# Performance work log

Measured on AMD Instinct MI355X. Metric: run time of the kernel, lower is better.

## Reference

```python
import jax, jax.numpy as jnp
import numpy as np

N, E = 50000, 800000
HID, EDGE_DIM, HEADS = 128, 16, 4
C = HID // HEADS  # 32
NEG_SLOPE = 0.2  # GATv2Conv default negative_slope


def setup_inputs() -> dict:
    key = jax.random.key(0)
    ks = jax.random.split(key, 16)
    def glorot(k, shape):
        fan_in = shape[0]
        return jax.random.normal(k, shape, jnp.float32) / np.sqrt(fan_in)
    return {
        "x": jax.random.normal(ks[0], (N, HID), jnp.float32),
        "edge_index": jax.random.randint(ks[1], (2, E), 0, N, jnp.int64 if jax.config.jax_enable_x64 else jnp.int32),
        "edge_attr": jax.random.normal(ks[2], (E, EDGE_DIM), jnp.float32),
        # GATv2Conv params (lin_l, lin_r with bias; lin_edge bias-free; att; final bias)
        "Wl": glorot(ks[3], (HID, HID)),
        "bl": jnp.zeros((HID,), jnp.float32),
        "Wr": glorot(ks[4], (HID, HID)),
        "br": jnp.zeros((HID,), jnp.float32),
        "We": glorot(ks[5], (EDGE_DIM, HID)),
        "att": glorot(ks[6], (HEADS, C)),
        "bias_gat": jnp.zeros((HID,), jnp.float32),
        # RMSNorm weights
        "w_norm1": jnp.ones((HID,), jnp.float32),
        "w_norm2": jnp.ones((HID,), jnp.float32),
        # FFN params
        "ffn_w1": glorot(ks[7], (HID, 4 * HID)),
        "ffn_b1": jnp.zeros((4 * HID,), jnp.float32),
        "ffn_w2": glorot(ks[8], (4 * HID, HID)),
        "ffn_b2": jnp.zeros((HID,), jnp.float32),
    }


def rmsnorm(x, w):
    # torch.nn.RMSNorm with eps=None -> eps = finfo(dtype).eps
    eps = jnp.finfo(x.dtype).eps
    ms = jnp.mean(x * x, axis=-1, keepdims=True)
    return x * jax.lax.rsqrt(ms + eps) * w


def gatv2_conv(x, edge_index, edge_attr, Wl, bl, Wr, br, We, att, bias_gat):
    n = x.shape[0]
    h, c = att.shape
    xl = (x @ Wl + bl).reshape(n, h, c)   # source-side transform (x_j)
    xr = (x @ Wr + br).reshape(n, h, c)   # target-side transform (x_i)
    src, dst = edge_index[0], edge_index[1]
    e = (edge_attr @ We).reshape(-1, h, c)
    m = xl[src] + xr[dst] + e                       # [E, H, C] per-edge message pre-activation
    s = jnp.where(m > 0, m, NEG_SLOPE * m)          # LeakyReLU(0.2)
    logits = jnp.einsum('ehc,hc->eh', s, att)       # [E, H]
    # scatter-softmax over edges grouped by target node
    lmax = jax.ops.segment_max(logits, dst, num_segments=n)
    ex = jnp.exp(logits - lmax[dst])
    den = jax.ops.segment_sum(ex, dst, num_segments=n)
    alpha = ex / (den[dst] + 1e-16)                 # PyG softmax denominator guard
    out = jax.ops.segment_sum(alpha[..., None] * xl[src], dst, num_segments=n)
    return out.reshape(n, h * c) + bias_gat


def reference(x, edge_index, edge_attr, Wl, bl, Wr, br, We, att, bias_gat,
              w_norm1, w_norm2, ffn_w1, ffn_b1, ffn_w2, ffn_b2):
    x_attn = gatv2_conv(x, edge_index, edge_attr, Wl, bl, Wr, br, We, att, bias_gat)
    h = rmsnorm(x + x_attn, w_norm1)
    f = jax.nn.gelu(h @ ffn_w1 + ffn_b1, approximate=False) @ ffn_w2 + ffn_b2
    return rmsnorm(h + f, w_norm2)
```

## Files before the change

### kernel.cpp

```cpp
#include <hip/hip_runtime.h>

#define NN 50000
#define EE 800000

typedef unsigned short u16;

#define OFF_GAT  0u
#define OFF_XLB  6400000u
#define OFF_XRB  9600000u
#define OFF_SE   12800000u
#define OFF_CNT  14400000u
#define OFF_OFS  14450000u
#define OFF_H    6400000u
#define OFF_HB   12800000u
#define OFF_WLRT 16000000u
#define OFF_W1T  16016384u
#define OFF_W2T  16049152u

#define RMS_EPS 1.1920928955078125e-7f

typedef float f32x4v __attribute__((ext_vector_type(4)));
typedef short s16x8 __attribute__((ext_vector_type(8)));

__device__ __forceinline__ f32x4v mfma16(s16x8 a, s16x8 b, f32x4v c) {
  return __builtin_amdgcn_mfma_f32_16x16x32_bf16(a, b, c, 0, 0, 0);
}
__device__ __forceinline__ u16 f2b(float f) {
  unsigned int u = __float_as_uint(f);
  unsigned int r = (u + 0x7fffu + ((u >> 16) & 1u)) >> 16;
  return (u16)r;
}
__device__ __forceinline__ float b2f(u16 u) {
  union { float f; unsigned int i; } x; x.i = ((unsigned int)u) << 16; return x.f;
}
__device__ __forceinline__ s16x8 ld_bf16x8_f32(const float* __restrict__ p) {
  float4 v0 = *(const float4*)p;
  float4 v1 = *(const float4*)(p + 4);
  s16x8 r;
  r[0] = (short)f2b(v0.x); r[1] = (short)f2b(v0.y);
  r[2] = (short)f2b(v0.z); r[3] = (short)f2b(v0.w);
  r[4] = (short)f2b(v1.x); r[5] = (short)f2b(v1.y);
  r[6] = (short)f2b(v1.z); r[7] = (short)f2b(v1.w);
  return r;
}
__device__ __forceinline__ float readlane_f32(float v, int lane) {
  return __int_as_float(__builtin_amdgcn_readlane(__float_as_int(v), lane));
}
__device__ __forceinline__ int readlane_i32(int v, int lane) {
  return __builtin_amdgcn_readlane(v, lane);
}
__device__ __forceinline__ float gelu_fast(float x) {
  float x2 = x * x;
  float y = x * fmaf(0.07135481283f, x2, 1.5957691216f);
  float e = __expf(-y);
  return x * __builtin_amdgcn_rcpf(1.0f + e);
}

__global__ __launch_bounds__(256) void k_prep(const float* __restrict__ Wl, const float* __restrict__ Wr,
    const float* __restrict__ W1, const float* __restrict__ W2,
    int* __restrict__ cnt, u16* __restrict__ wlrt, u16* __restrict__ w1t, u16* __restrict__ w2t)
{
  int i = blockIdx.x * 256 + threadIdx.x;
  if (i < NN) cnt[i] = 0;
  if (i < 32768) {
    int n = i >> 7, k = i & 127;
    float v = (n < 128) ? Wl[k * 128 + n] : Wr[k * 128 + (n - 128)];
    wlrt[i] = f2b(v);
  }
  {
    int n = i >> 7, k = i & 127;
    w1t[i] = f2b(W1[k * 512 + n]);
  }
  {
    int n = i >> 9, k = i & 511;
    w2t[i] = f2b(W2[k * 128 + n]);
  }
}

__global__ __launch_bounds__(256) void k_hist(const int* __restrict__ ei, int* __restrict__ cnt) {
  int e = blockIdx.x * 256 + threadIdx.x;
  if (e < EE) atomicAdd(&cnt[ei[EE + e]], 1);
}

__global__ __launch_bounds__(1024) void k_scan(const int* __restrict__ cnt,
    int* __restrict__ offs, int* __restrict__ pos)
{
  __shared__ int wsum[16];
  __shared__ int carry_s;
  int tid = threadIdx.x, lane = tid & 63, wv = tid >> 6;
  if (tid == 0) carry_s = 0;
  __syncthreads();
  for (int base = 0; base < NN; base += 1024) {
    int i = base + tid;
    int v = (i < NN) ? cnt[i] : 0;
    int x = v;
#pragma unroll
    for (int ofs = 1; ofs < 64; ofs <<= 1) {
      int y = __shfl_up(x, ofs);
      if (lane >= ofs) x += y;
    }
    if (lane == 63) wsum[wv] = x;
    __syncthreads();
    if (wv == 0) {
      int s = (lane < 16) ? wsum[lane] : 0;
#pragma unroll
      for (int ofs = 1; ofs < 16; ofs <<= 1) {
        int y = __shfl_up(s, ofs);
        if (lane >= ofs) s += y;
      }
      if (lane < 16) wsum[lane] = s;
    }
    __syncthreads();
    int wbase = (wv > 0) ? wsum[wv - 1] : 0;
    int incl = x + wbase + carry_s;
    if (i < NN) { offs[i + 1] = incl; pos[i] = incl - v; }
    if (base == 0 && tid == 0) offs[0] = 0;
    __syncthreads();
    if (tid == 1023) carry_s = incl;
    __syncthreads();
  }
}

__global__ __launch_bounds__(256) void k_permute(const int* __restrict__ ei,
    int* __restrict__ pos, int2* __restrict__ se)
{
  int e = blockIdx.x * 256 + threadIdx.x;
  if (e < EE) {
    int slot = atomicAdd(&pos[ei[EE + e]], 1);
    se[slot] = make_int2(ei[e], e);
  }
}

__global__ __launch_bounds__(256) void k1_mfma(const float* __restrict__ x, const u16* __restrict__ wlrt,
    const float* __restrict__ bl, const float* __restrict__ br,
    u16* __restrict__ xlb, u16* __restrict__ xrb)
{
  int tid = threadIdx.x;
  int w = tid >> 6, lane = tid & 63;
  int quad = lane >> 4, l16 = lane & 15;
  int row0 = blockIdx.x * 32;
  int ko = quad * 8;
  f32x4v acc[2][4];
#pragma unroll
  for (int mt = 0; mt < 2; ++mt)
#pragma unroll
    for (int nt = 0; nt < 4; ++nt) acc[mt][nt] = (f32x4v){0.f, 0.f, 0.f, 0.f};
#pragma unroll
  for (int ks = 0; ks < 4; ++ks) {
    int k0 = ks * 32 + ko;
    s16x8 a[2];
#pragma unroll
    for (int mt = 0; mt < 2; ++mt) {
      int row = row0 + mt * 16 + l16; if (row >= NN) row = NN - 1;
      a[mt] = ld_bf16x8_f32(x + row * 128 + k0);
    }
#pragma unroll
    for (int nt = 0; nt < 4; ++nt) {
      int col = w * 64 + nt * 16 + l16;
      s16x8 b = *(const s16x8*)(wlrt + col * 128 + k0);
      acc[0][nt] = mfma16(a[0], b, acc[0][nt]);
      acc[1][nt] = mfma16(a[1], b, acc[1][nt]);
    }
  }
#pragma unroll
  for (int nt = 0; nt < 4; ++nt) {
    int col = w * 64 + nt * 16 + l16;
    bool isl = col < 128;
    float bias = isl ? bl[col] : br[col - 128];
    u16* dst = isl ? xlb : xrb;
    int cc = isl ? col : col - 128;
#pragma unroll
    for (int mt = 0; mt < 2; ++mt)
#pragma unroll
      for (int r = 0; r < 4; ++r) {
        int row = row0 + mt * 16 + quad * 4 + r;
        if (row < NN) dst[row * 128 + cc] = f2b(acc[mt][nt][r] + bias);
      }
  }
}

__global__ __launch_bounds__(256) void k2_attn(
    const int* __restrict__ offs, const int2* __restrict__ se,
    const float* __restrict__ eattr,
    const float* __restrict__ att, const float* __restrict__ We,
    const u16* __restrict__ xlb, const u16* __restrict__ xrb,
    float* __restrict__ gat)
{
  int l = threadIdx.x & 63;
  int wid = (blockIdx.x * blockDim.x + threadIdx.x) >> 6;
  int nw = (gridDim.x * blockDim.x) >> 6;
  int c0 = 2 * l;
  const float2* We2 = (const float2*)We;
  float2 wef[16];
#pragma unroll
  for (int k = 0; k < 16; ++k) wef[k] = We2[k * 64 + l];
  float a0 = att[c0], a1 = att[c0 + 1];
  for (int d = wid; d < NN; d += nw) {
    int start = offs[d];
    int deg = offs[d + 1] - start;
    ushort2 xru = *(const ushort2*)(xrb + d * 128 + c0);
    float xr0 = b2f(xru.x), xr1 = b2f(xru.y);
    float mh = -1e30f, lh = 0.f, O0 = 0.f, O1 = 0.f;
    for (int base = 0; base < deg; base += 64) {
      bool act = (base + l) < deg;
      int idx = start + base + l;
      int2 sev = act ? se[idx] : make_int2(0, 0);
      int cnt = min(64, deg - base);
      for (int sub = 0; sub < cnt; sub += 4) {
        int eidq = __shfl(sev.y, sub + (l >> 4));
        float eav = eattr[eidq * 16 + (l & 15)];
        float p[4], xl0v[4], xl1v[4];
#pragma unroll
        for (int j2 = 0; j2 < 4; ++j2) {
          float ep0 = 0.f, ep1 = 0.f;
#pragma unroll
          for (int k = 0; k < 16; ++k) {
            float ek = readlane_f32(eav, j2 * 16 + k);
            ep0 = fmaf(ek, wef[k].x, ep0);
            ep1 = fmaf(ek, wef[k].y, ep1);
          }
          int sr = readlane_i32(sev.x, sub + j2);
          ushort2 xlu = *(const ushort2*)(xlb + sr * 128 + c0);
          float xl0 = b2f(xlu.x), xl1 = b2f(xlu.y);
          float m0 = xl0 + xr0 + ep0;
          float m1 = xl1 + xr1 + ep1;
          float s0 = m0 > 0.f ? m0 : 0.2f * m0;
          float s1 = m1 > 0.f ? m1 : 0.2f * m1;
          p[j2] = fmaf(s0, a0, s1 * a1);
          xl0v[j2] = xl0; xl1v[j2] = xl1;
        }
#pragma unroll
        for (int o = 1; o <= 8; o <<= 1) {
          p[0] += __shfl_xor(p[0], o);
          p[1] += __shfl_xor(p[1], o);
          p[2] += __shfl_xor(p[2], o);
          p[3] += __shfl_xor(p[3], o);
        }
#pragma unroll
        for (int j2 = 0; j2 < 4; ++j2) if (sub + j2 >= cnt) p[j2] = -1e30f;
        float nm = fmaxf(fmaxf(fmaxf(p[0], p[1]), fmaxf(p[2], p[3])), mh);
        float sc = __expf(mh - nm);
        float w0 = __expf(p[0] - nm), w1 = __expf(p[1] - nm);
        float w2 = __expf(p[2] - nm), w3 = __expf(p[3] - nm);
        lh = fmaf(lh, sc, (w0 + w1) + (w2 + w3));
        O0 = fmaf(O0, sc, fmaf(w0, xl0v[0], fmaf(w1, xl0v[1], fmaf(w2, xl0v[2], w3 * xl0v[3]))));
        O1 = fmaf(O1, sc, fmaf(w0, xl1v[0], fmaf(w1, xl1v[1], fmaf(w2, xl1v[2], w3 * xl1v[3]))));
        mh = nm;
      }
    }
    float inv = 1.f / (lh + 1e-16f);
    *(float2*)(gat + d * 128 + c0) = make_float2(O0 * inv, O1 * inv);
  }
}

__global__ __launch_bounds__(256) void k5_norm1(const float* __restrict__ x,
    const float* __restrict__ gat, const float* __restrict__ bg,
    const float* __restrict__ wn1, float* __restrict__ h, u16* __restrict__ hb)
{
  int l = threadIdx.x & 63;
  int row = blockIdx.x * 4 + (threadIdx.x >> 6);
  int c0 = 2 * l;
  float2 xu = *(const float2*)(x + row * 128 + c0);
  float2 gv = *(const float2*)(gat + row * 128 + c0);
  float2 bu = *(const float2*)(bg + c0);
  float v0 = xu.x + gv.x + bu.x;
  float v1 = xu.y + gv.y + bu.y;
  float ss = v0 * v0 + v1 * v1;
#pragma unroll
  for (int o = 1; o < 64; o <<= 1) ss += __shfl_xor(ss, o);
  float rr = rsqrtf(ss * (1.f / 128.f) + RMS_EPS);
  float2 wu = *(const float2*)(wn1 + c0);
  float o0 = v0 * rr * wu.x, o1 = v1 * rr * wu.y;
  *(float2*)(h + row * 128 + c0) = make_float2(o0, o1);
  ushort2 hu; hu.x = f2b(o0); hu.y = f2b(o1);
  *(ushort2*)(hb + row * 128 + c0) = hu;
}

__device__ __forceinline__ u16* tls_addr(u16* tls, int row, int col) {
  int byte = (row << 10) + (col << 1);
  byte ^= (row & 7) << 4;
  return (u16*)((char*)tls + byte);
}

__global__ __launch_bounds__(512) void k6_mfma(const float* __restrict__ h,
    const u16* __restrict__ hb,
    const u16* __restrict__ w1t, const u16* __restrict__ w2t,
    const float* __restrict__ b1, const float* __restrict__ b2,
    const float* __restrict__ wn2, float* __restrict__ out)
{
  __shared__ u16 tls[32 * 512];
  int tid = threadIdx.x;
  int w = tid >> 6, lane = tid & 63;
  int quad = lane >> 4, l16 = lane & 15;
  int row0 = blockIdx.x * 32;
  int ko = quad * 8;

  f32x4v acc1[2][4];
#pragma unroll
  for (int mt = 0; mt < 2; ++mt)
#pragma unroll
    for (int nt = 0; nt < 4; ++nt) acc1[mt][nt] = (f32x4v){0.f, 0.f, 0.f, 0.f};
#pragma unroll
  for (int ks = 0; ks < 4; ++ks) {
    int k0 = ks * 32 + ko;
    s16x8 a[2];
#pragma unroll
    for (int mt = 0; mt < 2; ++mt) {
      int row = row0 + mt * 16 + l16; if (row >= NN) row = NN - 1;
      a[mt] = *(const s16x8*)(hb + row * 128 + k0);
    }
#pragma unroll
    for (int nt = 0; nt < 4; ++nt) {
      int col = w * 64 + nt * 16 + l16;
      s16x8 b = *(const s16x8*)(w1t + col * 128 + k0);
      acc1[0][nt] = mfma16(a[0], b, acc1[0][nt]);
      acc1[1][nt] = mfma16(a[1], b, acc1[1][nt]);
    }
  }
#pragma unroll
  for (int nt = 0; nt < 4; ++nt) {
    int col = w * 64 + nt * 16 + l16;
    float bb = b1[col];
#pragma unroll
    for (int mt = 0; mt < 2; ++mt)
#pragma unroll
      for (int r = 0; r < 4; ++r) {
        float t = gelu_fast(acc1[mt][nt][r] + bb);
        *tls_addr(tls, mt * 16 + quad * 4 + r, col) = f2b(t);
      }
  }
  __syncthreads();

  f32x4v acc2[2];
  acc2[0] = (f32x4v){0.f, 0.f, 0.f, 0.f};
  acc2[1] = (f32x4v){0.f, 0.f, 0.f, 0.f};
  int col = w * 16 + l16;
  const u16* bptr = w2t + col * 512;
#pragma unroll
  for (int ks = 0; ks < 16; ++ks) {
    int k0 = ks * 32 + ko;
    s16x8 a2[2];
#pragma unroll
    for (int mt = 0; mt < 2; ++mt)
      a2[mt] = *(const s16x8*)tls_addr(tls, mt * 16 + l16, k0);
    s16x8 b = *(const s16x8*)(bptr + k0);
    acc2[0] = mfma16(a2[0], b, acc2[0]);
    acc2[1] = mfma16(a2[1], b, acc2[1]);
  }

  float bb2 = b2[col], wn = wn2[col];
  float ov[2][4];
#pragma unroll
  for (int mt = 0; mt < 2; ++mt)
#pragma unroll
    for (int r = 0; r < 4; ++r) {
      int row = row0 + mt * 16 + quad * 4 + r;
      int rowc = row < NN ? row : NN - 1;
      ov[mt][r] = h[rowc * 128 + col] + acc2[mt][r] + bb2;
    }
  __syncthreads();
  float (*red)[32] = (float (*)[32])(void*)tls;
#pragma unroll
  for (int mt = 0; mt < 2; ++mt)
#pragma unroll
    for (int r = 0; r < 4; ++r) {
      float q = ov[mt][r] * ov[mt][r];
      q += __shfl_xor(q, 1); q += __shfl_xor(q, 2);
      q += __shfl_xor(q, 4); q += __shfl_xor(q, 8);
      if (l16 == 0) red[w][mt * 16 + quad * 4 + r] = q;
    }
  __syncthreads();
#pragma unroll
  for (int mt = 0; mt < 2; ++mt)
#pragma unroll
    for (int r = 0; r < 4; ++r) {
      int rl = mt * 16 + quad * 4 + r;
      float tot = ((red[0][rl] + red[1][rl]) + (red[2][rl] + red[3][rl]))
                + ((red[4][rl] + red[5][rl]) + (red[6][rl] + red[7][rl]));
      float rr = rsqrtf(tot * (1.f / 128.f) + RMS_EPS);
      int row = row0 + rl;
      if (row < NN) out[row * 128 + col] = ov[mt][r] * rr * wn;
    }
}

extern "C" void kernel_launch(void* const* d_in, const int* in_sizes, int n_in,
                              void* d_out, int out_size, void* d_ws, size_t ws_size,
                              hipStream_t stream) {
  const float* x   = (const float*)d_in[0];
  const int*   ei  = (const int*)d_in[1];
  const float* ea  = (const float*)d_in[2];
  const float* Wl  = (const float*)d_in[3];
  const float* bl  = (const float*)d_in[4];
  const float* Wr  = (const float*)d_in[5];
  const float* br  = (const float*)d_in[6];
  const float* We  = (const float*)d_in[7];
  const float* att = (const float*)d_in[8];
  const float* bg  = (const float*)d_in[9];
  const float* wn1 = (const float*)d_in[10];
  const float* wn2 = (const float*)d_in[11];
  const float* W1  = (const float*)d_in[12];
  const float* b1  = (const float*)d_in[13];
  const float* W2  = (const float*)d_in[14];
  const float* b2  = (const float*)d_in[15];

  float* wsf = (float*)d_ws;
  int*   wsi = (int*)d_ws;

  float* gat  = wsf + OFF_GAT;
  u16* xlb    = (u16*)(wsf + OFF_XLB);
  u16* xrb    = (u16*)(wsf + OFF_XRB);
  int2* se    = (int2*)(wsf + OFF_SE);
  int* cnt    = wsi + OFF_CNT;
  int* pos    = wsi + OFF_CNT;
  int* offs   = wsi + OFF_OFS;
  float* hbuf = wsf + OFF_H;
  u16* hb     = (u16*)(wsf + OFF_HB);
  u16* wlrt   = (u16*)(wsf + OFF_WLRT);
  u16* w1t    = (u16*)(wsf + OFF_W1T);
  u16* w2t    = (u16*)(wsf + OFF_W2T);

  k_prep<<<256, 256, 0, stream>>>(Wl, Wr, W1, W2, cnt, wlrt, w1t, w2t);

  k_hist<<<(EE + 255) / 256, 256, 0, stream>>>(ei, cnt);
  k_scan<<<1, 1024, 0, stream>>>(cnt, offs, pos);
  k_permute<<<(EE + 255) / 256, 256, 0, stream>>>(ei, pos, se);

  k1_mfma<<<(NN + 31) / 32, 256, 0, stream>>>(x, wlrt, bl, br, xlb, xrb);

  k2_attn<<<2048, 256, 0, stream>>>(offs, se, ea, att, We, xlb, xrb, gat);

  k5_norm1<<<NN / 4, 256, 0, stream>>>(x, gat, bg, wn1, hbuf, hb);

  k6_mfma<<<(NN + 31) / 32, 512, 0, stream>>>(hbuf, hb, w1t, w2t, b1, b2, wn2, (float*)d_out);
}
```

Before: 514.8 us.

## Compute edge-attribute projection with MFMA into per-wave LDS in attention kernel

The per-edge projection edge_attr@We moves off a scalar readlane/FMA loop and onto bf16 MFMA, 16 edges at a time. Results are staged in a per-wave shared-memory buffer and read back in the softmax-aggregation loop. This removes many readlane and FMA instructions per edge. In exchange it rounds edge_attr and We to bf16, adds LDS traffic and 32KB of shared memory per block, and halves the attention grid size.

```diff
diff --git a/kernel.cpp b/kernel.cpp
--- a/kernel.cpp
+++ b/kernel.cpp
@@ -43,9 +43,6 @@
   r[6] = (short)f2b(v1.z); r[7] = (short)f2b(v1.w);
   return r;
 }
-__device__ __forceinline__ float readlane_f32(float v, int lane) {
-  return __int_as_float(__builtin_amdgcn_readlane(__float_as_int(v), lane));
-}
 __device__ __forceinline__ int readlane_i32(int v, int lane) {
   return __builtin_amdgcn_readlane(v, lane);
 }
@@ -186,15 +183,32 @@
     const u16* __restrict__ xlb, const u16* __restrict__ xrb,
     float* __restrict__ gat)
 {
+  __shared__ float epbuf[4][16 * 128];
   int l = threadIdx.x & 63;
+  int wv = threadIdx.x >> 6;
+  int l16 = l & 15, quad = l >> 4;
   int wid = (blockIdx.x * blockDim.x + threadIdx.x) >> 6;
   int nw = (gridDim.x * blockDim.x) >> 6;
   int c0 = 2 * l;
-  const float2* We2 = (const float2*)We;
-  float2 wef[16];
-#pragma unroll
-  for (int k = 0; k < 16; ++k) wef[k] = We2[k * 64 + l];
+  float* epl = epbuf[wv];
+
+  s16x8 bfrag[8];
+  {
+    bool kz = quad >= 2;
+    int kb = (quad & 1) * 8;
+#pragma unroll
+    for (int t = 0; t < 8; ++t) {
+      s16x8 b;
+#pragma unroll
+      for (int e = 0; e < 8; ++e) {
+        float v = kz ? 0.f : We[(kb + e) * 128 + t * 16 + l16];
+        b[e] = (short)f2b(v);
+      }
+      bfrag[t] = b;
+    }
+  }
   float a0 = att[c0], a1 = att[c0 + 1];
+
   for (int d = wid; d < NN; d += nw) {
     int start = offs[d];
     int deg = offs[d + 1] - start;
@@ -206,46 +220,51 @@
       int idx = start + base + l;
       int2 sev = act ? se[idx] : make_int2(0, 0);
       int cnt = min(64, deg - base);
-      for (int sub = 0; sub < cnt; sub += 4) {
-        int eidq = __shfl(sev.y, sub + (l >> 4));
-        float eav = eattr[eidq * 16 + (l & 15)];
-        float p[4], xl0v[4], xl1v[4];
-#pragma unroll
-        for (int j2 = 0; j2 < 4; ++j2) {
-          float ep0 = 0.f, ep1 = 0.f;
-#pragma unroll
-          for (int k = 0; k < 16; ++k) {
-            float ek = readlane_f32(eav, j2 * 16 + k);
-            ep0 = fmaf(ek, wef[k].x, ep0);
-            ep1 = fmaf(ek, wef[k].y, ep1);
+      for (int sub16 = 0; sub16 < cnt; sub16 += 16) {
+        int eidv = __shfl(sev.y, sub16 + l16);
+        s16x8 afrag = ld_bf16x8_f32(eattr + (size_t)eidv * 16 + (quad & 1) * 8);
+#pragma unroll
+        for (int t = 0; t < 8; ++t) {
+          f32x4v ac = mfma16(afrag, bfrag[t], (f32x4v){0.f, 0.f, 0.f, 0.f});
+          int cb = t * 16 + l16;
+#pragma unroll
+          for (int r = 0; r < 4; ++r)
+            epl[(quad * 4 + r) * 128 + cb] = ac[r];
+        }
+        int cend = min(sub16 + 16, cnt);
+        for (int sub = sub16; sub < cend; sub += 4) {
+          float p[4], xl0v[4], xl1v[4];
+#pragma unroll
+          for (int j2 = 0; j2 < 4; ++j2) {
+            int sr = readlane_i32(sev.x, sub + j2);
+            float2 epv = *(const float2*)&epl[(sub - sub16 + j2) * 128 + c0];
+            ushort2 xlu = *(const ushort2*)(xlb + (size_t)sr * 128 + c0);
+            float xl0 = b2f(xlu.x), xl1 = b2f(xlu.y);
+            float m0 = xl0 + xr0 + epv.x;
+            float m1 = xl1 + xr1 + epv.y;
+            float s0 = m0 > 0.f ? m0 : 0.2f * m0;
+            float s1 = m1 > 0.f ? m1 : 0.2f * m1;
+            p[j2] = fmaf(s0, a0, s1 * a1);
+            xl0v[j2] = xl0; xl1v[j2] = xl1;
           }
-          int sr = readlane_i32(sev.x, sub + j2);
-          ushort2 xlu = *(const ushort2*)(xlb + sr * 128 + c0);
-          float xl0 = b2f(xlu.x), xl1 = b2f(xlu.y);
-          float m0 = xl0 + xr0 + ep0;
-          float m1 = xl1 + xr1 + ep1;
-          float s0 = m0 > 0.f ? m0 : 0.2f * m0;
-          float s1 = m1 > 0.f ? m1 : 0.2f * m1;
-          p[j2] = fmaf(s0, a0, s1 * a1);
-          xl0v[j2] = xl0; xl1v[j2] = xl1;
+#pragma unroll
+          for (int o = 1; o <= 8; o <<= 1) {
+            p[0] += __shfl_xor(p[0], o);
+            p[1] += __shfl_xor(p[1], o);
+            p[2] += __shfl_xor(p[2], o);
+            p[3] += __shfl_xor(p[3], o);
+          }
+#pragma unroll
+          for (int j2 = 0; j2 < 4; ++j2) if (sub + j2 >= cnt) p[j2] = -1e30f;
+          float nm = fmaxf(fmaxf(fmaxf(p[0], p[1]), fmaxf(p[2], p[3])), mh);
+          float sc = __expf(mh - nm);
+          float w0 = __expf(p[0] - nm), w1 = __expf(p[1] - nm);
+          float w2 = __expf(p[2] - nm), w3 = __expf(p[3] - nm);
+          lh = fmaf(lh, sc, (w0 + w1) + (w2 + w3));
+          O0 = fmaf(O0, sc, fmaf(w0, xl0v[0], fmaf(w1, xl0v[1], fmaf(w2, xl0v[2], w3 * xl0v[3]))));
+          O1 = fmaf(O1, sc, fmaf(w0, xl1v[0], fmaf(w1, xl1v[1], fmaf(w2, xl1v[2], w3 * xl1v[3]))));
+          mh = nm;
         }
-#pragma unroll
-        for (int o = 1; o <= 8; o <<= 1) {
-          p[0] += __shfl_xor(p[0], o);
-          p[1] += __shfl_xor(p[1], o);
-          p[2] += __shfl_xor(p[2], o);
-          p[3] += __shfl_xor(p[3], o);
-        }
-#pragma unroll
-        for (int j2 = 0; j2 < 4; ++j2) if (sub + j2 >= cnt) p[j2] = -1e30f;
-        float nm = fmaxf(fmaxf(fmaxf(p[0], p[1]), fmaxf(p[2], p[3])), mh);
-        float sc = __expf(mh - nm);
-        float w0 = __expf(p[0] - nm), w1 = __expf(p[1] - nm);
-        float w2 = __expf(p[2] - nm), w3 = __expf(p[3] - nm);
-        lh = fmaf(lh, sc, (w0 + w1) + (w2 + w3));
-        O0 = fmaf(O0, sc, fmaf(w0, xl0v[0], fmaf(w1, xl0v[1], fmaf(w2, xl0v[2], w3 * xl0v[3]))));
-        O1 = fmaf(O1, sc, fmaf(w0, xl1v[0], fmaf(w1, xl1v[1], fmaf(w2, xl1v[2], w3 * xl1v[3]))));
-        mh = nm;
       }
     }
     float inv = 1.f / (lh + 1e-16f);
@@ -427,7 +446,7 @@
 
   k1_mfma<<<(NN + 31) / 32, 256, 0, stream>>>(x, wlrt, bl, br, xlb, xrb);
 
-  k2_attn<<<2048, 256, 0, stream>>>(offs, se, ea, att, We, xlb, xrb, gat);
+  k2_attn<<<1024, 256, 0, stream>>>(offs, se, ea, att, We, xlb, xrb, gat);
 
   k5_norm1<<<NN / 4, 256, 0, stream>>>(x, gat, bg, wn1, hbuf, hb);
 
```

Result: slower. 536.4 us (+4.2%).

## Use packed fp16 dot math in attention and fuse RMSNorm1 into attention

Applied to the files above, without the earlier changes.

Edge attributes are converted to packed fp16 in the histogram pass, and xl/xr are stored as fp16 instead of bf16. The attention kernel then computes edge projections and logits with packed fp16 dot2 and handles 8 edges per step. The first RMSNorm is folded into the attention epilogue, which removes the gat buffer and a separate kernel launch, and h is written into the output buffer in place. The FFN kernel now converts h from fp32 to bf16 on load instead of reading a bf16 copy, and the lower fp16 precision in the logit math may affect accuracy.

```diff
diff --git a/kernel.cpp b/kernel.cpp
--- a/kernel.cpp
+++ b/kernel.cpp
@@ -5,14 +5,12 @@
 
 typedef unsigned short u16;
 
-#define OFF_GAT  0u
-#define OFF_XLB  6400000u
-#define OFF_XRB  9600000u
+#define OFF_EAH  0u
+#define OFF_XLH  6400000u
+#define OFF_XRH  9600000u
 #define OFF_SE   12800000u
 #define OFF_CNT  14400000u
 #define OFF_OFS  14450000u
-#define OFF_H    6400000u
-#define OFF_HB   12800000u
 #define OFF_WLRT 16000000u
 #define OFF_W1T  16016384u
 #define OFF_W2T  16049152u
@@ -21,6 +19,8 @@
 
 typedef float f32x4v __attribute__((ext_vector_type(4)));
 typedef short s16x8 __attribute__((ext_vector_type(8)));
+typedef _Float16 h16x2 __attribute__((ext_vector_type(2)));
+typedef __fp16   g16x2 __attribute__((ext_vector_type(2)));
 
 __device__ __forceinline__ f32x4v mfma16(s16x8 a, s16x8 b, f32x4v c) {
   return __builtin_amdgcn_mfma_f32_16x16x32_bf16(a, b, c, 0, 0, 0);
@@ -30,10 +30,23 @@
   unsigned int r = (u + 0x7fffu + ((u >> 16) & 1u)) >> 16;
   return (u16)r;
 }
-__device__ __forceinline__ float b2f(u16 u) {
-  union { float f; unsigned int i; } x; x.i = ((unsigned int)u) << 16; return x.f;
-}
-__device__ __forceinline__ s16x8 ld_bf16x8_f32(const float* __restrict__ p) {
+__device__ __forceinline__ u16 f2h(float f) {
+  union { _Float16 h; u16 u; } x; x.h = (_Float16)f; return x.u;
+}
+__device__ __forceinline__ h16x2 pk(float a, float b) {
+  union { g16x2 g; h16x2 h; } u; u.g = __builtin_amdgcn_cvt_pkrtz(a, b); return u.h;
+}
+__device__ __forceinline__ h16x2 u2h(unsigned int u) {
+  union { unsigned int i; h16x2 h; } x; x.i = u; return x.h;
+}
+__device__ __forceinline__ unsigned int h2u(h16x2 h) {
+  union { unsigned int i; h16x2 h; } x; x.h = h; return x.i;
+}
+__device__ __forceinline__ float fdot2(h16x2 a, h16x2 b, float c) {
+  union { h16x2 h; g16x2 g; } ua, ub; ua.h = a; ub.h = b;
+  return __builtin_amdgcn_fdot2(ua.g, ub.g, c, false);
+}
+__device__ __forceinline__ s16x8 ld_bf16x8_f32(const float* p) {
   float4 v0 = *(const float4*)p;
   float4 v1 = *(const float4*)(p + 4);
   s16x8 r;
@@ -43,9 +56,6 @@
   r[6] = (short)f2b(v1.z); r[7] = (short)f2b(v1.w);
   return r;
 }
-__device__ __forceinline__ float readlane_f32(float v, int lane) {
-  return __int_as_float(__builtin_amdgcn_readlane(__float_as_int(v), lane));
-}
 __device__ __forceinline__ int readlane_i32(int v, int lane) {
   return __builtin_amdgcn_readlane(v, lane);
 }
@@ -77,9 +87,26 @@
   }
 }
 
-__global__ __launch_bounds__(256) void k_hist(const int* __restrict__ ei, int* __restrict__ cnt) {
+__global__ __launch_bounds__(256) void k_hist(const int* __restrict__ ei, const float* __restrict__ eattr,
+    int* __restrict__ cnt, unsigned int* __restrict__ eah)
+{
   int e = blockIdx.x * 256 + threadIdx.x;
-  if (e < EE) atomicAdd(&cnt[ei[EE + e]], 1);
+  if (e < EE) {
+    atomicAdd(&cnt[ei[EE + e]], 1);
+    const float4* src = (const float4*)(eattr + (size_t)e * 16);
+    float4 v0 = src[0], v1 = src[1], v2 = src[2], v3 = src[3];
+    uint4 o0, o1;
+    o0.x = h2u(pk(v0.x, v0.y));
+    o0.y = h2u(pk(v0.z, v0.w));
+    o0.z = h2u(pk(v1.x, v1.y));
+    o0.w = h2u(pk(v1.z, v1.w));
+    o1.x = h2u(pk(v2.x, v2.y));
+    o1.y = h2u(pk(v2.z, v2.w));
+    o1.z = h2u(pk(v3.x, v3.y));
+    o1.w = h2u(pk(v3.z, v3.w));
+    uint4* dst = (uint4*)(eah + (size_t)e * 8);
+    dst[0] = o0; dst[1] = o1;
+  }
 }
 
 __global__ __launch_bounds__(1024) void k_scan(const int* __restrict__ cnt,
@@ -133,7 +160,7 @@
 
 __global__ __launch_bounds__(256) void k1_mfma(const float* __restrict__ x, const u16* __restrict__ wlrt,
     const float* __restrict__ bl, const float* __restrict__ br,
-    u16* __restrict__ xlb, u16* __restrict__ xrb)
+    u16* __restrict__ xlh, u16* __restrict__ xrh)
 {
   int tid = threadIdx.x;
   int w = tid >> 6, lane = tid & 63;
@@ -167,113 +194,117 @@
     int col = w * 64 + nt * 16 + l16;
     bool isl = col < 128;
     float bias = isl ? bl[col] : br[col - 128];
-    u16* dst = isl ? xlb : xrb;
+    u16* dst = isl ? xlh : xrh;
     int cc = isl ? col : col - 128;
 #pragma unroll
     for (int mt = 0; mt < 2; ++mt)
 #pragma unroll
       for (int r = 0; r < 4; ++r) {
         int row = row0 + mt * 16 + quad * 4 + r;
-        if (row < NN) dst[row * 128 + cc] = f2b(acc[mt][nt][r] + bias);
+        if (row < NN) dst[row * 128 + cc] = f2h(acc[mt][nt][r] + bias);
       }
   }
 }
 
-__global__ __launch_bounds__(256) void k2_attn(
+__global__ __launch_bounds__(256) void kA_attn(
     const int* __restrict__ offs, const int2* __restrict__ se,
-    const float* __restrict__ eattr,
+    const unsigned int* __restrict__ eah,
     const float* __restrict__ att, const float* __restrict__ We,
-    const u16* __restrict__ xlb, const u16* __restrict__ xrb,
-    float* __restrict__ gat)
+    const u16* __restrict__ xlh, const u16* __restrict__ xrh,
+    const float* __restrict__ x, const float* __restrict__ bg,
+    const float* __restrict__ wn1, float* __restrict__ h)
 {
   int l = threadIdx.x & 63;
   int wid = (blockIdx.x * blockDim.x + threadIdx.x) >> 6;
   int nw = (gridDim.x * blockDim.x) >> 6;
   int c0 = 2 * l;
-  const float2* We2 = (const float2*)We;
-  float2 wef[16];
-#pragma unroll
-  for (int k = 0; k < 16; ++k) wef[k] = We2[k * 64 + l];
-  float a0 = att[c0], a1 = att[c0 + 1];
+
+  h16x2 wefA[8], wefB[8];
+#pragma unroll
+  for (int k = 0; k < 8; ++k) {
+    wefA[k] = pk(We[(2 * k) * 128 + c0], We[(2 * k + 1) * 128 + c0]);
+    wefB[k] = pk(We[(2 * k) * 128 + c0 + 1], We[(2 * k + 1) * 128 + c0 + 1]);
+  }
+  h16x2 att2 = pk(att[c0], att[c0 + 1]);
+  const h16x2 c06 = {(_Float16)0.6f, (_Float16)0.6f};
+  const h16x2 c04 = {(_Float16)0.4f, (_Float16)0.4f};
+
+  int myj = l >> 3, myk = l & 7;
+
   for (int d = wid; d < NN; d += nw) {
     int start = offs[d];
     int deg = offs[d + 1] - start;
-    ushort2 xru = *(const ushort2*)(xrb + d * 128 + c0);
-    float xr0 = b2f(xru.x), xr1 = b2f(xru.y);
+    h16x2 xr2 = u2h(*(const unsigned int*)(xrh + (size_t)d * 128 + c0));
     float mh = -1e30f, lh = 0.f, O0 = 0.f, O1 = 0.f;
+
     for (int base = 0; base < deg; base += 64) {
       bool act = (base + l) < deg;
       int idx = start + base + l;
       int2 sev = act ? se[idx] : make_int2(0, 0);
       int cnt = min(64, deg - base);
-      for (int sub = 0; sub < cnt; sub += 4) {
-        int eidq = __shfl(sev.y, sub + (l >> 4));
-        float eav = eattr[eidq * 16 + (l & 15)];
-        float p[4], xl0v[4], xl1v[4];
-#pragma unroll
-        for (int j2 = 0; j2 < 4; ++j2) {
+      for (int sub8 = 0; sub8 < cnt; sub8 += 8) {
+        int eidq = __shfl(sev.y, sub8 + myj);
+        unsigned int eav = eah[(size_t)eidq * 8 + myk];
+
+        float p[8];
+        unsigned int xlu[8];
+#pragma unroll
+        for (int j = 0; j < 8; ++j) {
           float ep0 = 0.f, ep1 = 0.f;
 #pragma unroll
-          for (int k = 0; k < 16; ++k) {
-            float ek = readlane_f32(eav, j2 * 16 + k);
-            ep0 = fmaf(ek, wef[k].x, ep0);
-            ep1 = fmaf(ek, wef[k].y, ep1);
+          for (int k = 0; k < 8; ++k) {
+            unsigned int ev = (unsigned int)readlane_i32((int)eav, j * 8 + k);
+            h16x2 e2 = u2h(ev);
+            ep0 = fdot2(e2, wefA[k], ep0);
+            ep1 = fdot2(e2, wefB[k], ep1);
           }
-          int sr = readlane_i32(sev.x, sub + j2);
-          ushort2 xlu = *(const ushort2*)(xlb + sr * 128 + c0);
-          float xl0 = b2f(xlu.x), xl1 = b2f(xlu.y);
-          float m0 = xl0 + xr0 + ep0;
-          float m1 = xl1 + xr1 + ep1;
-          float s0 = m0 > 0.f ? m0 : 0.2f * m0;
-          float s1 = m1 > 0.f ? m1 : 0.2f * m1;
-          p[j2] = fmaf(s0, a0, s1 * a1);
-          xl0v[j2] = xl0; xl1v[j2] = xl1;
+          int sr = readlane_i32(sev.x, sub8 + j);
+          unsigned int xv = *(const unsigned int*)(xlh + (size_t)sr * 128 + c0);
+          xlu[j] = xv;
+          h16x2 m2 = u2h(xv) + xr2 + pk(ep0, ep1);
+          h16x2 am = u2h(h2u(m2) & 0x7FFF7FFFu);
+          h16x2 s2 = m2 * c06 + am * c04;
+          p[j] = fdot2(s2, att2, 0.f);
         }
 #pragma unroll
         for (int o = 1; o <= 8; o <<= 1) {
-          p[0] += __shfl_xor(p[0], o);
-          p[1] += __shfl_xor(p[1], o);
-          p[2] += __shfl_xor(p[2], o);
-          p[3] += __shfl_xor(p[3], o);
+          p[0] += __shfl_xor(p[0], o); p[1] += __shfl_xor(p[1], o);
+          p[2] += __shfl_xor(p[2], o); p[3] += __shfl_xor(p[3], o);
+          p[4] += __shfl_xor(p[4], o); p[5] += __shfl_xor(p[5], o);
+          p[6] += __shfl_xor(p[6], o); p[7] += __shfl_xor(p[7], o);
         }
 #pragma unroll
-        for (int j2 = 0; j2 < 4; ++j2) if (sub + j2 >= cnt) p[j2] = -1e30f;
-        float nm = fmaxf(fmaxf(fmaxf(p[0], p[1]), fmaxf(p[2], p[3])), mh);
+        for (int j = 0; j < 8; ++j) if (sub8 + j >= cnt) p[j] = -1e30f;
+        float nm = fmaxf(fmaxf(fmaxf(p[0], p[1]), fmaxf(p[2], p[3])),
+                         fmaxf(fmaxf(p[4], p[5]), fmaxf(p[6], p[7])));
+        nm = fmaxf(nm, mh);
         float sc = __expf(mh - nm);
-        float w0 = __expf(p[0] - nm), w1 = __expf(p[1] - nm);
-        float w2 = __expf(p[2] - nm), w3 = __expf(p[3] - nm);
-        lh = fmaf(lh, sc, (w0 + w1) + (w2 + w3));
-        O0 = fmaf(O0, sc, fmaf(w0, xl0v[0], fmaf(w1, xl0v[1], fmaf(w2, xl0v[2], w3 * xl0v[3]))));
-        O1 = fmaf(O1, sc, fmaf(w0, xl1v[0], fmaf(w1, xl1v[1], fmaf(w2, xl1v[2], w3 * xl1v[3]))));
+#pragma unroll
+        for (int j = 0; j < 8; ++j) p[j] = __expf(p[j] - nm);
+        float bs = ((p[0] + p[1]) + (p[2] + p[3])) + ((p[4] + p[5]) + (p[6] + p[7]));
+        lh = fmaf(lh, sc, bs);
+        O0 *= sc; O1 *= sc;
         mh = nm;
+#pragma unroll
+        for (int j = 0; j < 8; ++j) {
+          h16x2 xl2 = u2h(xlu[j]);
+          O0 = fmaf(p[j], (float)xl2.x, O0);
+          O1 = fmaf(p[j], (float)xl2.y, O1);
+        }
       }
     }
     float inv = 1.f / (lh + 1e-16f);
-    *(float2*)(gat + d * 128 + c0) = make_float2(O0 * inv, O1 * inv);
-  }
-}
-
-__global__ __launch_bounds__(256) void k5_norm1(const float* __restrict__ x,
-    const float* __restrict__ gat, const float* __restrict__ bg,
-    const float* __restrict__ wn1, float* __restrict__ h, u16* __restrict__ hb)
-{
-  int l = threadIdx.x & 63;
-  int row = blockIdx.x * 4 + (threadIdx.x >> 6);
-  int c0 = 2 * l;
-  float2 xu = *(const float2*)(x + row * 128 + c0);
-  float2 gv = *(const float2*)(gat + row * 128 + c0);
-  float2 bu = *(const float2*)(bg + c0);
-  float v0 = xu.x + gv.x + bu.x;
-  float v1 = xu.y + gv.y + bu.y;
-  float ss = v0 * v0 + v1 * v1;
-#pragma unroll
-  for (int o = 1; o < 64; o <<= 1) ss += __shfl_xor(ss, o);
-  float rr = rsqrtf(ss * (1.f / 128.f) + RMS_EPS);
-  float2 wu = *(const float2*)(wn1 + c0);
-  float o0 = v0 * rr * wu.x, o1 = v1 * rr * wu.y;
-  *(float2*)(h + row * 128 + c0) = make_float2(o0, o1);
-  ushort2 hu; hu.x = f2b(o0); hu.y = f2b(o1);
-  *(ushort2*)(hb + row * 128 + c0) = hu;
+    float2 xu = *(const float2*)(x + (size_t)d * 128 + c0);
+    float2 bu = *(const float2*)(bg + c0);
+    float v0 = O0 * inv + xu.x + bu.x;
+    float v1 = O1 * inv + xu.y + bu.y;
+    float ss = v0 * v0 + v1 * v1;
+#pragma unroll
+    for (int o = 1; o < 64; o <<= 1) ss += __shfl_xor(ss, o);
+    float rr = rsqrtf(ss * (1.f / 128.f) + RMS_EPS);
+    float2 wu = *(const float2*)(wn1 + c0);
+    *(float2*)(h + (size_t)d * 128 + c0) = make_float2(v0 * rr * wu.x, v1 * rr * wu.y);
+  }
 }
 
 __device__ __forceinline__ u16* tls_addr(u16* tls, int row, int col) {
@@ -282,11 +313,10 @@
   return (u16*)((char*)tls + byte);
 }
 
-__global__ __launch_bounds__(512) void k6_mfma(const float* __restrict__ h,
-    const u16* __restrict__ hb,
+__global__ __launch_bounds__(512) void k6_mfma(const float* h,
     const u16* __restrict__ w1t, const u16* __restrict__ w2t,
     const float* __restrict__ b1, const float* __restrict__ b2,
-    const float* __restrict__ wn2, float* __restrict__ out)
+    const float* __restrict__ wn2, float* out)
 {
   __shared__ u16 tls[32 * 512];
   int tid = threadIdx.x;
@@ -307,7 +337,7 @@
 #pragma unroll
     for (int mt = 0; mt < 2; ++mt) {
       int row = row0 + mt * 16 + l16; if (row >= NN) row = NN - 1;
-      a[mt] = *(const s16x8*)(hb + row * 128 + k0);
+      a[mt] = ld_bf16x8_f32(h + row * 128 + k0);
     }
 #pragma unroll
     for (int nt = 0; nt < 4; ++nt) {
@@ -379,7 +409,9 @@
                 + ((red[4][rl] + red[5][rl]) + (red[6][rl] + red[7][rl]));
       float rr = rsqrtf(tot * (1.f / 128.f) + RMS_EPS);
       int row = row0 + rl;
-      if (row < NN) out[row * 128 + col] = ov[mt][r] * rr * wn;
+      if (row < NN) {
+        out[row * 128 + col] = ov[mt][r] * rr * wn;
+      }
     }
 }
 
@@ -406,30 +438,27 @@
   float* wsf = (float*)d_ws;
   int*   wsi = (int*)d_ws;
 
-  float* gat  = wsf + OFF_GAT;
-  u16* xlb    = (u16*)(wsf + OFF_XLB);
-  u16* xrb    = (u16*)(wsf + OFF_XRB);
+  unsigned int* eah = (unsigned int*)(wsf + OFF_EAH);
+  u16* xlh    = (u16*)(wsf + OFF_XLH);
+  u16* xrh    = (u16*)(wsf + OFF_XRH);
   int2* se    = (int2*)(wsf + OFF_SE);
   int* cnt    = wsi + OFF_CNT;
   int* pos    = wsi + OFF_CNT;
   int* offs   = wsi + OFF_OFS;
-  float* hbuf = wsf + OFF_H;
-  u16* hb     = (u16*)(wsf + OFF_HB);
   u16* wlrt   = (u16*)(wsf + OFF_WLRT);
   u16* w1t    = (u16*)(wsf + OFF_W1T);
   u16* w2t    = (u16*)(wsf + OFF_W2T);
+  float* hbuf = (float*)d_out;
 
   k_prep<<<256, 256, 0, stream>>>(Wl, Wr, W1, W2, cnt, wlrt, w1t, w2t);
 
-  k_hist<<<(EE + 255) / 256, 256, 0, stream>>>(ei, cnt);
+  k_hist<<<(EE + 255) / 256, 256, 0, stream>>>(ei, ea, cnt, eah);
   k_scan<<<1, 1024, 0, stream>>>(cnt, offs, pos);
   k_permute<<<(EE + 255) / 256, 256, 0, stream>>>(ei, pos, se);
 
-  k1_mfma<<<(NN + 31) / 32, 256, 0, stream>>>(x, wlrt, bl, br, xlb, xrb);
-
-  k2_attn<<<2048, 256, 0, stream>>>(offs, se, ea, att, We, xlb, xrb, gat);
-
-  k5_norm1<<<NN / 4, 256, 0, stream>>>(x, gat, bg, wn1, hbuf, hb);
-
-  k6_mfma<<<(NN + 31) / 32, 512, 0, stream>>>(hbuf, hb, w1t, w2t, b1, b2, wn2, (float*)d_out);
-}
+  k1_mfma<<<(NN + 31) / 32, 256, 0, stream>>>(x, wlrt, bl, br, xlh, xrh);
+
+  kA_attn<<<2048, 256, 0, stream>>>(offs, se, eah, att, We, xlh, xrh, x, bg, wn1, hbuf);
+
+  k6_mfma<<<(NN + 31) / 32, 512, 0, stream>>>(hbuf, w1t, w2t, b1, b2, wn2, (float*)d_out);
+}
```

Result: no change. 508.1 us (-1.3%).
